# Kernel optimization log

Hardware: AMD Instinct MI355X
Metric: run time of the kernel (lower is better)

The kernel has to match this reference:

```python
import jax, jax.numpy as jnp
import numpy as np

UNK_ID = 0
EPS = 1e-20


def setup_inputs() -> dict:
    key = jax.random.key(0)
    k1, k2, k3, k4, k5 = jax.random.split(key, 5)
    bs, ls, vocab, emb = 8, 256, 32000, 100
    return {
        "logits": jax.random.normal(k1, (bs, ls, vocab), dtype=jnp.float32),
        "gumbel_u": jax.random.uniform(k2, (bs, ls, vocab), dtype=jnp.float32),
        "inp_word": jax.random.randint(k3, (bs, ls), 0, vocab, dtype=jnp.int64),
        "obf_mask": jax.random.randint(k4, (bs, ls), 0, 2, dtype=jnp.int32),
        "parser_emb_weight": jax.random.normal(k5, (vocab, emb), dtype=jnp.float32),
    }


def reference(logits, gumbel_u, inp_word, obf_mask, parser_emb_weight):
    # dec ends in LogSoftmax -> gen_logits are log-probs
    lp = jax.nn.log_softmax(logits, axis=-1)                       # [b,s,V]
    mask = obf_mask.astype(bool)                                   # [b,s]
    vocab = lp.shape[-1]

    # ent_loss = mean over masked rows of lp * exp(lp)
    ent_all = jnp.sum(lp * jnp.exp(lp), axis=-1)                   # [b,s]
    n_masked = jnp.sum(mask).astype(lp.dtype)
    ent_loss = jnp.sum(jnp.where(mask, ent_all, 0.0)) / (n_masked * vocab)

    # gumbel_softmax(targeted_logits, temperature=1.0) -- eval mode
    g = -jnp.log(-jnp.log(gumbel_u + EPS) + EPS)
    relaxed = jax.nn.softmax(lp + g, axis=-1)                      # [b,s,V]
    sampled_idx = jnp.argmax(relaxed, axis=-1)                     # [b,s]
    sampled_emb = jnp.einsum('bsv,vd->bsd', relaxed, parser_emb_weight)

    # masked_scatter_ chains collapse to per-position selects:
    #   masked & safe   -> sampled_idx / sampled_emb
    #   masked & unsafe -> UNK_ID / W[UNK_ID]
    #   unmasked        -> inp_word / W[inp_word]
    safe = sampled_idx != inp_word                                 # [b,s]
    obf_word = jnp.where(mask, jnp.where(safe, sampled_idx, UNK_ID), inp_word)
    base_emb = parser_emb_weight[inp_word]                         # [b,s,d]
    unk_emb = parser_emb_weight[UNK_ID]                            # [d]
    obf_word_emb = jnp.where(
        mask[..., None],
        jnp.where(safe[..., None], sampled_emb, unk_emb),
        base_emb,
    )
    return obf_word, obf_word_emb, ent_loss
```

## Files before the change

### kernel.cpp

```cpp
#include <hip/hip_runtime.h>

#define P_TOT   2048
#define V       32000
#define D       100
#define DPAD    128
#define TS      32
#define VSPLIT  10
#define KB      3200
#define VC      128
#define NCHUNK  25
#define ASTRIDE 136
#define BSTRIDE 136

typedef __attribute__((ext_vector_type(8))) short short8;
typedef __attribute__((ext_vector_type(4))) float floatx4;

static __device__ __forceinline__ unsigned short f2bf(float x) {
    unsigned u = __float_as_uint(x);
    u += 0x7FFFu + ((u >> 16) & 1u);
    return (unsigned short)(u >> 16);
}

__global__ __launch_bounds__(256)
void k_prep(const float* __restrict__ W, unsigned short* __restrict__ Wt) {
    __shared__ float tile[64 * 133];
    const int vb = blockIdx.x * 64;
    const int tid = threadIdx.x;
    #pragma unroll
    for (int it = 0; it < 32; ++it) {
        int idx = it * 256 + tid;
        int d = idx & 127, vl = idx >> 7;
        float val = (d < D) ? W[(size_t)(vb + vl) * D + d] : 0.0f;
        tile[vl * 133 + d] = val;
    }
    __syncthreads();
    #pragma unroll
    for (int it = 0; it < 32; ++it) {
        int idx = it * 256 + tid;
        int vl = idx & 63, d = idx >> 6;
        Wt[(size_t)d * V + vb + vl] = f2bf(tile[vl * 133 + d]);
    }
}

__global__ __launch_bounds__(256, 3)
void k_main(const float* __restrict__ logits, const float* __restrict__ gum,
            const unsigned short* __restrict__ Wt,
            float* __restrict__ Epart, float* __restrict__ stats) {
    __shared__ unsigned short Abuf[TS * ASTRIDE];
    __shared__ unsigned short Bbuf[DPAD * BSTRIDE];
    __shared__ __align__(16) float alphaS[TS];
    __shared__ float m2run[TS], s2run[TS], amaxv[TS];
    __shared__ int amaxi[TS];

    const int tid   = threadIdx.x;
    const int r     = tid >> 3;
    const int q     = tid & 7;
    const int lane  = tid & 63;
    const int w     = tid >> 6;
    const int mtile = w & 1;
    const int ngrp  = w >> 1;
    const int stile = blockIdx.x;
    const int vs    = blockIdx.y;

    const int grow = stile * TS + r;
    const size_t rowbase = (size_t)grow * V + (size_t)vs * KB;

    if (q == 0) {
        m2run[r] = -1e30f; s2run[r] = 0.0f;
        amaxv[r] = -1e30f; amaxi[r] = 0;
    }
    float m1 = -1e30f, sA = 0.0f, sB = 0.0f;
    floatx4 acc[4];
    #pragma unroll
    for (int i = 0; i < 4; ++i) acc[i] = (floatx4){0.f, 0.f, 0.f, 0.f};

    for (int ch = 0; ch < NCHUNK; ++ch) {
        __syncthreads();
        const int cbase = ch * VC;

        {
            const unsigned short* src = Wt + (size_t)vs * KB + cbase;
            #pragma unroll
            for (int it = 0; it < 8; ++it) {
                int idx = it * 256 + tid;
                int dd = idx >> 4, seg = idx & 15;
                uint4 vwt = *(const uint4*)(src + (size_t)dd * V + seg * 8);
                *(uint4*)(&Bbuf[dd * BSTRIDE + seg * 8]) = vwt;
            }
        }

        float lg[16], zz[16];
        {
            const float* lptr = logits + rowbase + cbase + q * 4;
            const float* uptr = gum    + rowbase + cbase + q * 4;
            float4 l4[4], u4[4];
            #pragma unroll
            for (int k = 0; k < 4; ++k) l4[k] = *(const float4*)(lptr + (size_t)k * 32);
            #pragma unroll
            for (int k = 0; k < 4; ++k) u4[k] = *(const float4*)(uptr + (size_t)k * 32);
            #pragma unroll
            for (int k = 0; k < 4; ++k) {
                lg[k*4+0] = l4[k].x; lg[k*4+1] = l4[k].y;
                lg[k*4+2] = l4[k].z; lg[k*4+3] = l4[k].w;
                float uu[4] = {u4[k].x, u4[k].y, u4[k].z, u4[k].w};
                #pragma unroll
                for (int l = 0; l < 4; ++l) {
                    float g = -logf(-logf(uu[l] + 1e-20f) + 1e-20f);
                    zz[k*4+l] = lg[k*4+l] + g;
                }
            }
        }

        {
            float cm = lg[0];
            #pragma unroll
            for (int j = 1; j < 16; ++j) cm = fmaxf(cm, lg[j]);
            float m1n = fmaxf(m1, cm);
            float sc = __expf(m1 - m1n);
            sB = (sB + sA * (m1 - m1n)) * sc;
            sA = sA * sc;
            m1 = m1n;
            #pragma unroll
            for (int j = 0; j < 16; ++j) {
                float t = lg[j] - m1;
                float e = __expf(t);
                sA += e; sB += t * e;
            }
        }

        float cmv = -1e30f; int cmi = 0;
        #pragma unroll
        for (int k = 0; k < 4; ++k)
            #pragma unroll
            for (int l = 0; l < 4; ++l) {
                int j = k*4 + l;
                int gidx = vs * KB + cbase + k*32 + q*4 + l;
                if (zz[j] > cmv) { cmv = zz[j]; cmi = gidx; }
            }
        #pragma unroll
        for (int m = 1; m < 8; m <<= 1) {
            float ov = __shfl_xor(cmv, m, 64);
            int   oi = __shfl_xor(cmi, m, 64);
            if (ov > cmv || (ov == cmv && oi < cmi)) { cmv = ov; cmi = oi; }
        }

        float m2old = m2run[r];
        float m2new = fmaxf(m2old, cmv);
        float csum = 0.0f;
        unsigned short pb[16];
        #pragma unroll
        for (int j = 0; j < 16; ++j) {
            float p = __expf(zz[j] - m2new);
            csum += p;
            pb[j] = f2bf(p);
        }
        #pragma unroll
        for (int k = 0; k < 4; ++k) {
            ushort4 v4 = make_ushort4(pb[k*4], pb[k*4+1], pb[k*4+2], pb[k*4+3]);
            *(ushort4*)(&Abuf[r * ASTRIDE + k*32 + q*4]) = v4;
        }
        #pragma unroll
        for (int m = 1; m < 8; m <<= 1) csum += __shfl_xor(csum, m, 64);
        if (q == 0) {
            float al = __expf(m2old - m2new);
            alphaS[r] = al;
            s2run[r] = s2run[r] * al + csum;
            m2run[r] = m2new;
            if (cmv > amaxv[r]) { amaxv[r] = cmv; amaxi[r] = cmi; }
        }

        __syncthreads();

        floatx4 al4 = *(const floatx4*)(&alphaS[mtile*16 + ((lane >> 4) << 2)]);
        #pragma unroll
        for (int nt = 0; nt < 4; ++nt) {
            acc[nt][0] *= al4[0]; acc[nt][1] *= al4[1];
            acc[nt][2] *= al4[2]; acc[nt][3] *= al4[3];
        }
        const int ka0 = (lane >> 4) << 3;
        const unsigned short* arow = &Abuf[(mtile*16 + (lane & 15)) * ASTRIDE + ka0];
        #pragma unroll
        for (int ks = 0; ks < 4; ++ks) {
            short8 a = *(const short8*)(arow + ks * 32);
            #pragma unroll
            for (int nt = 0; nt < 4; ++nt) {
                const unsigned short* brow =
                    &Bbuf[(ngrp*64 + nt*16 + (lane & 15)) * BSTRIDE + ka0 + ks*32];
                short8 b = *(const short8*)brow;
                acc[nt] = __builtin_amdgcn_mfma_f32_16x16x32_bf16(a, b, acc[nt], 0, 0, 0);
            }
        }
    }

    #pragma unroll
    for (int m = 1; m < 8; m <<= 1) {
        float om = __shfl_xor(m1, m, 64);
        float oA = __shfl_xor(sA, m, 64);
        float oB = __shfl_xor(sB, m, 64);
        float mn = fmaxf(m1, om);
        float ea = __expf(m1 - mn), eb = __expf(om - mn);
        sB = (sB + sA * (m1 - mn)) * ea + (oB + oA * (om - mn)) * eb;
        sA = sA * ea + oA * eb;
        m1 = mn;
    }
    if (q == 0) {
        float* st = stats + ((size_t)grow * VSPLIT + vs) * 8;
        st[0] = m1; st[1] = sA; st[2] = sB;
        st[3] = m2run[r]; st[4] = s2run[r];
        st[5] = amaxv[r]; st[6] = __int_as_float(amaxi[r]); st[7] = 0.0f;
    }
    #pragma unroll
    for (int nt = 0; nt < 4; ++nt) {
        int n = ngrp*64 + nt*16 + (lane & 15);
        if (n < D) {
            #pragma unroll
            for (int i = 0; i < 4; ++i) {
                int row = mtile*16 + ((lane >> 4) << 2) + i;
                int pos = stile * TS + row;
                Epart[((size_t)pos * VSPLIT + vs) * D + n] = acc[nt][i];
            }
        }
    }
}

__global__ __launch_bounds__(128)
void k_combine(const float* __restrict__ stats, const float* __restrict__ Epart,
               const float* __restrict__ W, const int* __restrict__ inp,
               const int* __restrict__ msk, float* __restrict__ out,
               float* __restrict__ entbuf) {
    const int pos = blockIdx.x;
    const int t = threadIdx.x;
    const float* st = stats + (size_t)pos * VSPLIT * 8;

    float m1 = -1e30f, sA = 0.0f, sB = 0.0f, m2g = -1e30f;
    float bestv = -1e30f; int besti = 0;
    #pragma unroll
    for (int p = 0; p < VSPLIT; ++p) {
        const float* s = st + p * 8;
        float om = s[0], oA = s[1], oB = s[2];
        float mn = fmaxf(m1, om);
        float ea = __expf(m1 - mn), eb = __expf(om - mn);
        sB = (sB + sA * (m1 - mn)) * ea + (oB + oA * (om - mn)) * eb;
        sA = sA * ea + oA * eb;
        m1 = mn;
        m2g = fmaxf(m2g, s[3]);
        float av = s[5];
        if (av > bestv) { bestv = av; besti = __float_as_int(s[6]); }
    }
    float beta[VSPLIT];
    float s2g = 0.0f;
    #pragma unroll
    for (int p = 0; p < VSPLIT; ++p) {
        beta[p] = __expf(st[p*8 + 3] - m2g);
        s2g += st[p*8 + 4] * beta[p];
    }

    const int iw = inp[pos];
    const bool mk = msk[pos] != 0;
    const bool safe = besti != iw;

    if (t == 0) {
        int obf = mk ? (safe ? besti : 0) : iw;
        out[pos] = (float)obf;
        float ent = sB / sA - logf(sA);
        entbuf[pos] = mk ? ent : 0.0f;
    }
    if (t < D) {
        float e = 0.0f;
        const float* ep = Epart + (size_t)pos * VSPLIT * D + t;
        #pragma unroll
        for (int p = 0; p < VSPLIT; ++p) e += ep[(size_t)p * D] * beta[p];
        e /= s2g;
        float val;
        if (mk) val = safe ? e : W[t];
        else    val = W[(size_t)iw * D + t];
        out[P_TOT + (size_t)pos * D + t] = val;
    }
}

__global__ __launch_bounds__(256)
void k_final(const float* __restrict__ entbuf, const int* __restrict__ msk,
             float* __restrict__ out) {
    __shared__ float se[4], sm[4];
    const int t = threadIdx.x;
    float e = 0.0f, m = 0.0f;
    for (int i = t; i < P_TOT; i += 256) {
        e += entbuf[i];
        m += (float)msk[i];
    }
    #pragma unroll
    for (int k = 32; k >= 1; k >>= 1) {
        e += __shfl_down(e, k, 64);
        m += __shfl_down(m, k, 64);
    }
    if ((t & 63) == 0) { se[t >> 6] = e; sm[t >> 6] = m; }
    __syncthreads();
    if (t == 0) {
        float te = se[0] + se[1] + se[2] + se[3];
        float tm = sm[0] + sm[1] + sm[2] + sm[3];
        out[P_TOT + (size_t)P_TOT * D] = te / (tm * (float)V);
    }
}

extern "C" void kernel_launch(void* const* d_in, const int* in_sizes, int n_in,
                              void* d_out, int out_size, void* d_ws, size_t ws_size,
                              hipStream_t stream) {
    const float* logits = (const float*)d_in[0];
    const float* gum    = (const float*)d_in[1];
    const int*   inp    = (const int*)d_in[2];
    const int*   msk    = (const int*)d_in[3];
    const float* W      = (const float*)d_in[4];
    float* out = (float*)d_out;

    char* ws = (char*)d_ws;
    unsigned short* Wt  = (unsigned short*)ws;
    float* Epart  = (float*)(ws + 8192000);
    float* stats  = (float*)(ws + 16384000);
    float* entbuf = (float*)(ws + 17039360);

    k_prep<<<500, 256, 0, stream>>>(W, Wt);
    dim3 g1(P_TOT / TS, VSPLIT);
    k_main<<<g1, 256, 0, stream>>>(logits, gum, Wt, Epart, stats);
    k_combine<<<P_TOT, 128, 0, stream>>>(stats, Epart, W, inp, msk, out, entbuf);
    k_final<<<1, 256, 0, stream>>>(entbuf, msk, out);
}
```

Before: 593.6 us.

## Pre-tile W into padded LDS images, use direct global-to-LDS loads, halve row tile

k_prep now writes W as bf16 tiles already laid out with the padded LDS stride, one tile per (vsplit, chunk), so k_main can copy each tile with global_load_lds straight into shared memory instead of going through registers. The row tile shrinks from 32 to 16 with 16 threads per row, occupancy hint rises to 4 blocks, and the logits and gumbel loads for the next chunk are issued one chunk ahead. The intent is to cut B-tile staging cost and hide the streaming-load latency of the large input arrays. In exchange, W tiles are re-read twice as often because there are twice as many row blocks, and each wave now does fewer MFMAs per shared-memory load.

Measured after the change: 578.4 us. -2.6%, faster.

```diff
diff --git a/kernel.cpp b/kernel.cpp
--- a/kernel.cpp
+++ b/kernel.cpp
@@ -4,13 +4,14 @@
 #define V       32000
 #define D       100
 #define DPAD    128
-#define TS      32
+#define TS      16
 #define VSPLIT  10
 #define KB      3200
 #define VC      128
 #define NCHUNK  25
 #define ASTRIDE 136
 #define BSTRIDE 136
+#define BTILE_BYTES (DPAD * BSTRIDE * 2)
 
 typedef __attribute__((ext_vector_type(8))) short short8;
 typedef __attribute__((ext_vector_type(4))) float floatx4;
@@ -21,107 +22,126 @@
     return (unsigned short)(u >> 16);
 }
 
+static __device__ __forceinline__ void gload_lds16(const void* g, void* l) {
+    __builtin_amdgcn_global_load_lds(
+        (const __attribute__((address_space(1))) unsigned int*)g,
+        (__attribute__((address_space(3))) unsigned int*)l, 16, 0, 0);
+}
+
 __global__ __launch_bounds__(256)
-void k_prep(const float* __restrict__ W, unsigned short* __restrict__ Wt) {
-    __shared__ float tile[64 * 133];
-    const int vb = blockIdx.x * 64;
+void k_prep(const float* __restrict__ W, unsigned short* __restrict__ Wtp) {
+    __shared__ float tile[VC * 101];
+    const int ch = blockIdx.x, vs = blockIdx.y;
+    const int vbase = vs * KB + ch * VC;
     const int tid = threadIdx.x;
-    #pragma unroll
-    for (int it = 0; it < 32; ++it) {
-        int idx = it * 256 + tid;
-        int d = idx & 127, vl = idx >> 7;
-        float val = (d < D) ? W[(size_t)(vb + vl) * D + d] : 0.0f;
-        tile[vl * 133 + d] = val;
+    const float* src = W + (size_t)vbase * D;
+    for (int idx = tid; idx < VC * D; idx += 256) {
+        int vl = idx / D, d = idx - vl * D;
+        tile[vl * 101 + d] = src[idx];
     }
     __syncthreads();
-    #pragma unroll
-    for (int it = 0; it < 32; ++it) {
-        int idx = it * 256 + tid;
-        int vl = idx & 63, d = idx >> 6;
-        Wt[(size_t)d * V + vb + vl] = f2bf(tile[vl * 133 + d]);
-    }
-}
-
-__global__ __launch_bounds__(256, 3)
+    unsigned short* dst = Wtp + (size_t)(vs * NCHUNK + ch) * (DPAD * BSTRIDE);
+    for (int idx = tid; idx < DPAD * BSTRIDE; idx += 256) {
+        int d = idx / BSTRIDE, e = idx - d * BSTRIDE;
+        float v = (d < D && e < VC) ? tile[e * 101 + d] : 0.0f;
+        dst[idx] = f2bf(v);
+    }
+}
+
+__global__ __launch_bounds__(256, 4)
 void k_main(const float* __restrict__ logits, const float* __restrict__ gum,
-            const unsigned short* __restrict__ Wt,
+            const unsigned short* __restrict__ Wtp,
             float* __restrict__ Epart, float* __restrict__ stats) {
-    __shared__ unsigned short Abuf[TS * ASTRIDE];
-    __shared__ unsigned short Bbuf[DPAD * BSTRIDE];
+    __shared__ __align__(16) unsigned short Abuf[TS * ASTRIDE];
+    __shared__ __align__(16) unsigned short Bbuf[DPAD * BSTRIDE];
     __shared__ __align__(16) float alphaS[TS];
     __shared__ float m2run[TS], s2run[TS], amaxv[TS];
     __shared__ int amaxi[TS];
 
     const int tid   = threadIdx.x;
-    const int r     = tid >> 3;
-    const int q     = tid & 7;
+    const int r     = tid >> 4;
+    const int q     = tid & 15;
     const int lane  = tid & 63;
     const int w     = tid >> 6;
-    const int mtile = w & 1;
-    const int ngrp  = w >> 1;
     const int stile = blockIdx.x;
     const int vs    = blockIdx.y;
 
     const int grow = stile * TS + r;
     const size_t rowbase = (size_t)grow * V + (size_t)vs * KB;
 
-    if (q == 0) {
-        m2run[r] = -1e30f; s2run[r] = 0.0f;
-        amaxv[r] = -1e30f; amaxi[r] = 0;
-    }
+    if (tid < TS) {
+        m2run[tid] = -1e30f; s2run[tid] = 0.0f;
+        amaxv[tid] = -1e30f; amaxi[tid] = 0;
+    }
+
     float m1 = -1e30f, sA = 0.0f, sB = 0.0f;
-    floatx4 acc[4];
-    #pragma unroll
-    for (int i = 0; i < 4; ++i) acc[i] = (floatx4){0.f, 0.f, 0.f, 0.f};
+    floatx4 acc[2];
+    acc[0] = (floatx4){0.f, 0.f, 0.f, 0.f};
+    acc[1] = (floatx4){0.f, 0.f, 0.f, 0.f};
+
+    const float* lbase = logits + rowbase + q * 8;
+    const float* ubase = gum    + rowbase + q * 8;
+
+    float4 cl0 = *(const float4*)(lbase);
+    float4 cl1 = *(const float4*)(lbase + 4);
+    float4 cu0 = *(const float4*)(ubase);
+    float4 cu1 = *(const float4*)(ubase + 4);
+
+    const char* wsrc = (const char*)Wtp + (size_t)vs * NCHUNK * BTILE_BYTES
+                     + (size_t)lane * 16;
 
     for (int ch = 0; ch < NCHUNK; ++ch) {
+        const int cbase = ch * VC;
+
         __syncthreads();
-        const int cbase = ch * VC;
 
         {
-            const unsigned short* src = Wt + (size_t)vs * KB + cbase;
+            const char* src = wsrc + (size_t)ch * BTILE_BYTES;
+            char* dstb = (char*)Bbuf;
             #pragma unroll
             for (int it = 0; it < 8; ++it) {
-                int idx = it * 256 + tid;
-                int dd = idx >> 4, seg = idx & 15;
-                uint4 vwt = *(const uint4*)(src + (size_t)dd * V + seg * 8);
-                *(uint4*)(&Bbuf[dd * BSTRIDE + seg * 8]) = vwt;
-            }
-        }
-
-        float lg[16], zz[16];
+                int k = it * 4 + w;
+                gload_lds16(src + k * 1024, dstb + k * 1024);
+            }
+            if (w < 2) {
+                int k = 32 + w;
+                gload_lds16(src + k * 1024, dstb + k * 1024);
+            }
+        }
+
+        float4 nl0, nl1, nu0, nu1;
+        if (ch + 1 < NCHUNK) {
+            const float* lp = lbase + cbase + VC;
+            const float* up = ubase + cbase + VC;
+            nl0 = *(const float4*)(lp);
+            nl1 = *(const float4*)(lp + 4);
+            nu0 = *(const float4*)(up);
+            nu1 = *(const float4*)(up + 4);
+        }
+
+        float lg[8], zz[8];
         {
-            const float* lptr = logits + rowbase + cbase + q * 4;
-            const float* uptr = gum    + rowbase + cbase + q * 4;
-            float4 l4[4], u4[4];
-            #pragma unroll
-            for (int k = 0; k < 4; ++k) l4[k] = *(const float4*)(lptr + (size_t)k * 32);
-            #pragma unroll
-            for (int k = 0; k < 4; ++k) u4[k] = *(const float4*)(uptr + (size_t)k * 32);
-            #pragma unroll
-            for (int k = 0; k < 4; ++k) {
-                lg[k*4+0] = l4[k].x; lg[k*4+1] = l4[k].y;
-                lg[k*4+2] = l4[k].z; lg[k*4+3] = l4[k].w;
-                float uu[4] = {u4[k].x, u4[k].y, u4[k].z, u4[k].w};
-                #pragma unroll
-                for (int l = 0; l < 4; ++l) {
-                    float g = -logf(-logf(uu[l] + 1e-20f) + 1e-20f);
-                    zz[k*4+l] = lg[k*4+l] + g;
-                }
+            float la[8] = {cl0.x, cl0.y, cl0.z, cl0.w, cl1.x, cl1.y, cl1.z, cl1.w};
+            float ua[8] = {cu0.x, cu0.y, cu0.z, cu0.w, cu1.x, cu1.y, cu1.z, cu1.w};
+            #pragma unroll
+            for (int j = 0; j < 8; ++j) {
+                lg[j] = la[j];
+                float g = -logf(-logf(ua[j] + 1e-20f) + 1e-20f);
+                zz[j] = la[j] + g;
             }
         }
 
         {
             float cm = lg[0];
             #pragma unroll
-            for (int j = 1; j < 16; ++j) cm = fmaxf(cm, lg[j]);
+            for (int j = 1; j < 8; ++j) cm = fmaxf(cm, lg[j]);
             float m1n = fmaxf(m1, cm);
             float sc = __expf(m1 - m1n);
             sB = (sB + sA * (m1 - m1n)) * sc;
             sA = sA * sc;
             m1 = m1n;
             #pragma unroll
-            for (int j = 0; j < 16; ++j) {
+            for (int j = 0; j < 8; ++j) {
                 float t = lg[j] - m1;
                 float e = __expf(t);
                 sA += e; sB += t * e;
@@ -130,15 +150,12 @@
 
         float cmv = -1e30f; int cmi = 0;
         #pragma unroll
-        for (int k = 0; k < 4; ++k)
-            #pragma unroll
-            for (int l = 0; l < 4; ++l) {
-                int j = k*4 + l;
-                int gidx = vs * KB + cbase + k*32 + q*4 + l;
-                if (zz[j] > cmv) { cmv = zz[j]; cmi = gidx; }
-            }
-        #pragma unroll
-        for (int m = 1; m < 8; m <<= 1) {
+        for (int j = 0; j < 8; ++j) {
+            int gidx = vs * KB + cbase + q * 8 + j;
+            if (zz[j] > cmv) { cmv = zz[j]; cmi = gidx; }
+        }
+        #pragma unroll
+        for (int m = 1; m < 16; m <<= 1) {
             float ov = __shfl_xor(cmv, m, 64);
             int   oi = __shfl_xor(cmi, m, 64);
             if (ov > cmv || (ov == cmv && oi < cmi)) { cmv = ov; cmi = oi; }
@@ -147,20 +164,17 @@
         float m2old = m2run[r];
         float m2new = fmaxf(m2old, cmv);
         float csum = 0.0f;
-        unsigned short pb[16];
-        #pragma unroll
-        for (int j = 0; j < 16; ++j) {
+        unsigned short pb[8];
+        #pragma unroll
+        for (int j = 0; j < 8; ++j) {
             float p = __expf(zz[j] - m2new);
             csum += p;
             pb[j] = f2bf(p);
         }
-        #pragma unroll
-        for (int k = 0; k < 4; ++k) {
-            ushort4 v4 = make_ushort4(pb[k*4], pb[k*4+1], pb[k*4+2], pb[k*4+3]);
-            *(ushort4*)(&Abuf[r * ASTRIDE + k*32 + q*4]) = v4;
-        }
-        #pragma unroll
-        for (int m = 1; m < 8; m <<= 1) csum += __shfl_xor(csum, m, 64);
+        *(ushort4*)(&Abuf[r * ASTRIDE + q * 8])     = make_ushort4(pb[0], pb[1], pb[2], pb[3]);
+        *(ushort4*)(&Abuf[r * ASTRIDE + q * 8 + 4]) = make_ushort4(pb[4], pb[5], pb[6], pb[7]);
+        #pragma unroll
+        for (int m = 1; m < 16; m <<= 1) csum += __shfl_xor(csum, m, 64);
         if (q == 0) {
             float al = __expf(m2old - m2new);
             alphaS[r] = al;
@@ -171,29 +185,31 @@
 
         __syncthreads();
 
-        floatx4 al4 = *(const floatx4*)(&alphaS[mtile*16 + ((lane >> 4) << 2)]);
-        #pragma unroll
-        for (int nt = 0; nt < 4; ++nt) {
+        floatx4 al4 = *(const floatx4*)(&alphaS[(lane >> 4) << 2]);
+        #pragma unroll
+        for (int nt = 0; nt < 2; ++nt) {
             acc[nt][0] *= al4[0]; acc[nt][1] *= al4[1];
             acc[nt][2] *= al4[2]; acc[nt][3] *= al4[3];
         }
         const int ka0 = (lane >> 4) << 3;
-        const unsigned short* arow = &Abuf[(mtile*16 + (lane & 15)) * ASTRIDE + ka0];
+        const unsigned short* arow = &Abuf[(lane & 15) * ASTRIDE + ka0];
         #pragma unroll
         for (int ks = 0; ks < 4; ++ks) {
             short8 a = *(const short8*)(arow + ks * 32);
             #pragma unroll
-            for (int nt = 0; nt < 4; ++nt) {
+            for (int nt = 0; nt < 2; ++nt) {
                 const unsigned short* brow =
-                    &Bbuf[(ngrp*64 + nt*16 + (lane & 15)) * BSTRIDE + ka0 + ks*32];
+                    &Bbuf[(w * 32 + nt * 16 + (lane & 15)) * BSTRIDE + ka0 + ks * 32];
                 short8 b = *(const short8*)brow;
                 acc[nt] = __builtin_amdgcn_mfma_f32_16x16x32_bf16(a, b, acc[nt], 0, 0, 0);
             }
         }
-    }
-
-    #pragma unroll
-    for (int m = 1; m < 8; m <<= 1) {
+
+        if (ch + 1 < NCHUNK) { cl0 = nl0; cl1 = nl1; cu0 = nu0; cu1 = nu1; }
+    }
+
+    #pragma unroll
+    for (int m = 1; m < 16; m <<= 1) {
         float om = __shfl_xor(m1, m, 64);
         float oA = __shfl_xor(sA, m, 64);
         float oB = __shfl_xor(sB, m, 64);
@@ -210,12 +226,12 @@
         st[5] = amaxv[r]; st[6] = __int_as_float(amaxi[r]); st[7] = 0.0f;
     }
     #pragma unroll
-    for (int nt = 0; nt < 4; ++nt) {
-        int n = ngrp*64 + nt*16 + (lane & 15);
+    for (int nt = 0; nt < 2; ++nt) {
+        int n = w * 32 + nt * 16 + (lane & 15);
         if (n < D) {
             #pragma unroll
             for (int i = 0; i < 4; ++i) {
-                int row = mtile*16 + ((lane >> 4) << 2) + i;
+                int row = ((lane >> 4) << 2) + i;
                 int pos = stile * TS + row;
                 Epart[((size_t)pos * VSPLIT + vs) * D + n] = acc[nt][i];
             }
@@ -313,14 +329,14 @@
     float* out = (float*)d_out;
 
     char* ws = (char*)d_ws;
-    unsigned short* Wt  = (unsigned short*)ws;
-    float* Epart  = (float*)(ws + 8192000);
-    float* stats  = (float*)(ws + 16384000);
-    float* entbuf = (float*)(ws + 17039360);
-
-    k_prep<<<500, 256, 0, stream>>>(W, Wt);
+    unsigned short* Wtp = (unsigned short*)ws;
+    float* Epart  = (float*)(ws + 8704000);
+    float* stats  = (float*)(ws + 16896000);
+    float* entbuf = (float*)(ws + 17551360);
+
+    k_prep<<<dim3(NCHUNK, VSPLIT), 256, 0, stream>>>(W, Wtp);
     dim3 g1(P_TOT / TS, VSPLIT);
-    k_main<<<g1, 256, 0, stream>>>(logits, gum, Wt, Epart, stats);
+    k_main<<<g1, 256, 0, stream>>>(logits, gum, Wtp, Epart, stats);
     k_combine<<<P_TOT, 128, 0, stream>>>(stats, Epart, W, inp, msk, out, entbuf);
     k_final<<<1, 256, 0, stream>>>(entbuf, msk, out);
 }
```
